# Kernel optimization log

Measured on AMD Instinct MI355X. Metric: run time of the kernel, lower is better.

The kernel has to match this reference:

```python
import jax, jax.numpy as jnp
import numpy as np

B = 4096          # number of instance groups (images)
C = 81            # num_classes + 1 (fixed by the 81x81 prior_rel buffer)
D_K = 64
MAX_N = 128       # max instances per group


def setup_inputs() -> dict:
    key = jax.random.key(0)
    rng = np.random.default_rng(0)
    ni = rng.integers(1, MAX_N + 1, size=B)
    ni[0] = MAX_N  # pin the max so padded length is deterministic
    num_instances = jnp.asarray(ni, dtype=jnp.int32)
    total = int(ni.sum())
    ks = jax.random.split(key, 10)
    s_in = 1.0 / np.sqrt(C)
    s_dk = 1.0 / np.sqrt(D_K)
    return {
        'x': jax.random.normal(ks[0], (total, C), jnp.float32),
        'num_instances': num_instances,
        'prior_rel': jax.random.normal(ks[1], (C, C), jnp.float32) * s_in,
        'wq': jax.random.normal(ks[2], (C, D_K), jnp.float32) * s_in,
        'bq': jnp.zeros((D_K,), jnp.float32),
        'wk': jax.random.normal(ks[3], (C, D_K), jnp.float32) * s_in,
        'bk': jnp.zeros((D_K,), jnp.float32),
        'wv': jax.random.normal(ks[4], (C, D_K), jnp.float32) * s_in,
        'bv': jnp.zeros((D_K,), jnp.float32),
        'wu': jax.random.normal(ks[5], (D_K, C), jnp.float32) * s_dk,
        'bu': jnp.zeros((C,), jnp.float32),
    }


def reference(x, num_instances, prior_rel, wq, bq, wk, bk, wv, bv, wu, bu):
    # num_instances is static ragged metadata (the torch code keeps it as a
    # Python list), so it is safe to pull concrete ints from it here.
    ni = np.asarray(num_instances)
    Bn = ni.shape[0]
    M = int(ni.max())
    total = x.shape[0]

    counts = jnp.asarray(ni, jnp.int32)                      # [B]
    offsets = jnp.concatenate([jnp.zeros((1,), jnp.int32),
                               jnp.cumsum(counts)[:-1]])      # [B]
    pos = jnp.arange(M, dtype=jnp.int32)                      # [M]
    mask = pos[None, :] < counts[:, None]                     # [B, M] valid slots
    idx = offsets[:, None] + pos[None, :]                     # [B, M] flat gather idx
    idx_safe = jnp.where(mask, idx, 0)

    # pad: split x into ragged groups, zero-pad each to length M
    padded = x[idx_safe] * mask[:, :, None].astype(x.dtype)   # [B, M, C]

    q = padded @ wq + bq                                      # [B, M, d_k]
    k = padded @ wk + bk                                      # [B, M, d_k]
    v = (padded @ prior_rel) @ wv + bv                        # [B, M, d_k]

    scores = jnp.einsum('bmd,bnd->bmn', q, k) / jnp.sqrt(
        jnp.asarray(D_K, x.dtype))                            # [B, M, M]
    # mask padded KEY columns (queries on padded rows are dropped at unpad)
    scores = jnp.where(mask[:, None, :], scores, -jnp.inf)
    probs = jax.nn.softmax(scores, axis=2)
    out = jnp.einsum('bmn,bnd->bmd', probs, v)                # [B, M, d_k]
    out = out @ wu + bu                                       # [B, M, C]

    # unpad: scatter valid rows back to their ragged flat positions
    tgt = jnp.where(mask, idx, total)                         # dump pad rows past end
    flat = jnp.zeros((total + 1, out.shape[-1]), out.dtype)
    flat = flat.at[tgt.reshape(-1)].set(out.reshape(-1, out.shape[-1]))
    return flat[:total]
```

## Files before the change

### kernel.cpp

```cpp
#include <hip/hip_runtime.h>


typedef __attribute__((ext_vector_type(8))) short short8;
typedef __attribute__((ext_vector_type(4))) float f32x4;
typedef __attribute__((ext_vector_type(4))) short short4v;

constexpr int C  = 81;
constexpr int DK = 64;
constexpr int CP = 96;

constexpr int QK_STRIDE = 72;
constexpr int VT_STRIDE = 136;
constexpr int OFF_K  = 0;
constexpr int OFF_VT = 128 * QK_STRIDE;
constexpr int SMEM_TOT = OFF_VT + 64 * VT_STRIDE;

__device__ inline ushort f2b(float f) {
    uint u = __float_as_uint(f);
    uint r = (u + 0x7fffu + ((u >> 16) & 1u)) >> 16;
    return (ushort)r;
}
__device__ inline uint pack2bf(float a, float b) {
    return (uint)f2b(a) | ((uint)f2b(b) << 16);
}
__device__ inline uint shflu(uint v, int srcLane) {
    return (uint)__shfl((int)v, srcLane, 64);
}
union U8 { short8 s; uint u[4]; };

#define MFMA16(a, b, c) __builtin_amdgcn_mfma_f32_16x16x32_bf16((a), (b), (c), 0, 0, 0)

__global__ void scan_counts(const int* __restrict__ counts,
                            int* __restrict__ offsets, int n) {
    __shared__ int part[256];
    int tid = threadIdx.x;
    int per = (n + 255) >> 8;
    int base = tid * per;
    int s = 0;
    for (int i = 0; i < per; i++) {
        int idx = base + i;
        if (idx < n) s += counts[idx];
    }
    part[tid] = s;
    __syncthreads();
    for (int off = 1; off < 256; off <<= 1) {
        int v = (tid >= off) ? part[tid - off] : 0;
        __syncthreads();
        part[tid] += v;
        __syncthreads();
    }
    int run = (tid == 0) ? 0 : part[tid - 1];
    for (int i = 0; i < per; i++) {
        int idx = base + i;
        if (idx < n) { offsets[idx] = run; run += counts[idx]; }
    }
}

__global__ void prep_weights(const float* __restrict__ prior,
                             const float* __restrict__ wq, const float* __restrict__ wk,
                             const float* __restrict__ wv, const float* __restrict__ wu,
                             ushort* __restrict__ wqT, ushort* __restrict__ wkT,
                             ushort* __restrict__ wvT, ushort* __restrict__ wuT) {
    int idx = blockIdx.x * 256 + threadIdx.x;
    int sec = idx / (DK * CP);
    int i   = idx - sec * (DK * CP);
    if (sec == 0 || sec == 1) {
        int n = i / CP, k = i - (i / CP) * CP;
        const float* w = (sec == 0) ? wq : wk;
        ushort* dst    = (sec == 0) ? wqT : wkT;
        dst[n * CP + k] = (k < C) ? f2b(w[k * DK + n]) : (ushort)0;
    } else if (sec == 2) {
        int n = i / CP, k = i - (i / CP) * CP;
        float s = 0.f;
        if (k < C)
            for (int e = 0; e < C; e++) s = fmaf(prior[k * C + e], wv[e * DK + n], s);
        wvT[n * CP + k] = (k < C) ? f2b(s) : (ushort)0;
    } else {
        int n = i / DK, k = i - (i / DK) * DK;
        wuT[n * DK + k] = (n < C) ? f2b(wu[k * C + n]) : (ushort)0;
    }
}

__launch_bounds__(256, 4)
__global__ void ravnet_mfma(const float* __restrict__ x,
                            const int* __restrict__ counts,
                            const int* __restrict__ offsets,
                            const ushort* __restrict__ wqT, const ushort* __restrict__ wkT,
                            const ushort* __restrict__ wvT, const ushort* __restrict__ wuT,
                            const float* __restrict__ bq, const float* __restrict__ bk,
                            const float* __restrict__ bv, const float* __restrict__ bu,
                            float* __restrict__ out) {
    __shared__ __align__(16) ushort sm[SMEM_TOT];

    const int b    = blockIdx.x;
    const int N    = counts[b];
    const long off = offsets[b];
    const int tid  = threadIdx.x;
    const int lane = tid & 63;
    const int wave = tid >> 6;
    const int quad = lane >> 4;
    const int m16  = lane & 15;
    const int NT8  = (N + 15) >> 4;
    const int NT4  = (N + 31) >> 5;
    const float* xsrc = x + off * C;

    const int srcE = ((quad & 1) << 5) + m16;
    const int srcO = srcE + 16;
    const bool hi  = (quad >> 1) != 0;

    short8 aq[2][2];

    #pragma unroll
    for (int t = 0; t < 2; t++) {
        const int rt = wave + 4 * t;
        if (rt < NT8) {
            const int row  = rt * 16 + m16;
            const bool vrow = row < N;
            const float* xr = xsrc + (long)(vrow ? row : (N - 1)) * C;
            short8 ax[3];
            #pragma unroll
            for (int ks = 0; ks < 2; ks++) {
                const int c0 = ks * 32 + quad * 8;
                short8 a;
                #pragma unroll
                for (int e = 0; e < 8; e++) a[e] = (short)f2b(vrow ? xr[c0 + e] : 0.f);
                ax[ks] = a;
            }
            {
                const int c0 = 64 + quad * 8;
                short8 a;
                #pragma unroll
                for (int e = 0; e < 8; e++) {
                    const int c = c0 + e;
                    a[e] = (short)((vrow && c < C) ? f2b(xr[c]) : (ushort)0);
                }
                ax[2] = a;
            }
            uint qpk[4][2];
            #pragma unroll
            for (int nt = 0; nt < 4; nt++) {
                f32x4 acc = {0.f, 0.f, 0.f, 0.f};
                #pragma unroll
                for (int ks = 0; ks < 3; ks++)
                    acc = MFMA16(*(const short8*)(wqT + (nt * 16 + m16) * CP + ks * 32 + quad * 8),
                                 ax[ks], acc);
                const f32x4 b4 = *(const f32x4*)(bq + nt * 16 + quad * 4);
                qpk[nt][0] = pack2bf(acc[0] + b4[0], acc[1] + b4[1]);
                qpk[nt][1] = pack2bf(acc[2] + b4[2], acc[3] + b4[3]);
            }
            #pragma unroll
            for (int ks = 0; ks < 2; ks++) {
                uint a0 = shflu(qpk[2 * ks][0], srcE), b0 = shflu(qpk[2 * ks + 1][0], srcE);
                uint a1 = shflu(qpk[2 * ks][1], srcE), b1 = shflu(qpk[2 * ks + 1][1], srcE);
                uint a2 = shflu(qpk[2 * ks][0], srcO), b2 = shflu(qpk[2 * ks + 1][0], srcO);
                uint a3 = shflu(qpk[2 * ks][1], srcO), b3 = shflu(qpk[2 * ks + 1][1], srcO);
                U8 u;
                u.u[0] = hi ? b0 : a0;  u.u[1] = hi ? b1 : a1;
                u.u[2] = hi ? b2 : a2;  u.u[3] = hi ? b3 : a3;
                aq[t][ks] = u.s;
            }
            #pragma unroll
            for (int nt = 0; nt < 4; nt++) {
                f32x4 acc = {0.f, 0.f, 0.f, 0.f};
                #pragma unroll
                for (int ks = 0; ks < 3; ks++)
                    acc = MFMA16(*(const short8*)(wkT + (nt * 16 + m16) * CP + ks * 32 + quad * 8),
                                 ax[ks], acc);
                const f32x4 b4 = *(const f32x4*)(bk + nt * 16 + quad * 4);
                short4v pk4;
                #pragma unroll
                for (int r = 0; r < 4; r++) pk4[r] = (short)f2b(acc[r] + b4[r]);
                *(short4v*)(sm + OFF_K + (rt * 16 + m16) * QK_STRIDE + nt * 16 + quad * 4) = pk4;
            }
            #pragma unroll
            for (int nt = 0; nt < 4; nt++) {
                f32x4 acc = {0.f, 0.f, 0.f, 0.f};
                #pragma unroll
                for (int ks = 0; ks < 3; ks++)
                    acc = MFMA16(ax[ks],
                                 *(const short8*)(wvT + (nt * 16 + m16) * CP + ks * 32 + quad * 8),
                                 acc);
                const float bb = bv[nt * 16 + m16];
                short4v pk4;
                #pragma unroll
                for (int r = 0; r < 4; r++) pk4[r] = (short)f2b(acc[r] + bb);
                *(short4v*)(sm + OFF_VT + (nt * 16 + m16) * VT_STRIDE + rt * 16 + quad * 4) = pk4;
            }
        }
    }
    if (NT8 & 1) {
        const int R = NT8 * 16;
        const int d = tid >> 2, c4 = (tid & 3) << 2;
        short4v z = {0, 0, 0, 0};
        *(short4v*)(sm + OFF_VT + d * VT_STRIDE + R + c4) = z;
    }
    __syncthreads();

    constexpr float SCALE = 0.18033688011112042f;
    #pragma unroll
    for (int t = 0; t < 2; t++) {
        const int qt = wave + 4 * t;
        if (qt < NT8) {
            f32x4 sacc[8];
            #pragma unroll
            for (int ct = 0; ct < 8; ct++) {
                if (ct < NT8) {
                    f32x4 a = {0.f, 0.f, 0.f, 0.f};
                    #pragma unroll
                    for (int ks = 0; ks < 2; ks++) {
                        short8 kb = *(const short8*)(sm + OFF_K + (ct * 16 + m16) * QK_STRIDE +
                                                     ks * 32 + quad * 8);
                        a = MFMA16(kb, aq[t][ks], a);
                    }
                    sacc[ct] = a;
                }
            }
            float mr = -3e38f;
            #pragma unroll
            for (int ct = 0; ct < 8; ct++) if (ct < NT8) {
                #pragma unroll
                for (int r = 0; r < 4; r++) {
                    const bool valid = (ct * 16 + quad * 4 + r) < N;
                    float s = valid ? sacc[ct][r] * SCALE : -3e38f;
                    sacc[ct][r] = s;
                    mr = fmaxf(mr, s);
                }
            }
            mr = fmaxf(mr, __shfl_xor(mr, 16, 64));
            mr = fmaxf(mr, __shfl_xor(mr, 32, 64));
            float lr = 0.f;
            #pragma unroll
            for (int ct = 0; ct < 8; ct++) if (ct < NT8) {
                #pragma unroll
                for (int r = 0; r < 4; r++) {
                    float p = __builtin_exp2f(sacc[ct][r] - mr);
                    sacc[ct][r] = p;
                    lr += p;
                }
            }
            lr += __shfl_xor(lr, 16, 64);
            lr += __shfl_xor(lr, 32, 64);
            const float linv = 1.f / lr;
            uint pk[8][2];
            #pragma unroll
            for (int ct = 0; ct < 8; ct++) {
                if (ct < NT8) {
                    pk[ct][0] = pack2bf(sacc[ct][0], sacc[ct][1]);
                    pk[ct][1] = pack2bf(sacc[ct][2], sacc[ct][3]);
                } else {
                    pk[ct][0] = 0u; pk[ct][1] = 0u;
                }
            }
            short8 ap[4];
            #pragma unroll
            for (int kt = 0; kt < 4; kt++) {
                if (kt < NT4) {
                    uint a0 = shflu(pk[2 * kt][0], srcE), b0 = shflu(pk[2 * kt + 1][0], srcE);
                    uint a1 = shflu(pk[2 * kt][1], srcE), b1 = shflu(pk[2 * kt + 1][1], srcE);
                    uint a2 = shflu(pk[2 * kt][0], srcO), b2 = shflu(pk[2 * kt + 1][0], srcO);
                    uint a3 = shflu(pk[2 * kt][1], srcO), b3 = shflu(pk[2 * kt + 1][1], srcO);
                    U8 u;
                    u.u[0] = hi ? b0 : a0;  u.u[1] = hi ? b1 : a1;
                    u.u[2] = hi ? b2 : a2;  u.u[3] = hi ? b3 : a3;
                    ap[kt] = u.s;
                }
            }
            uint opk[4][2];
            #pragma unroll
            for (int ot = 0; ot < 4; ot++) {
                f32x4 oa = {0.f, 0.f, 0.f, 0.f};
                #pragma unroll
                for (int kt = 0; kt < 4; kt++) if (kt < NT4) {
                    short8 vb = *(const short8*)(sm + OFF_VT + (ot * 16 + m16) * VT_STRIDE +
                                                 kt * 32 + quad * 8);
                    oa = MFMA16(vb, ap[kt], oa);
                }
                opk[ot][0] = pack2bf(oa[0] * linv, oa[1] * linv);
                opk[ot][1] = pack2bf(oa[2] * linv, oa[3] * linv);
            }
            short8 ao[2];
            #pragma unroll
            for (int ks = 0; ks < 2; ks++) {
                uint a0 = shflu(opk[2 * ks][0], srcE), b0 = shflu(opk[2 * ks + 1][0], srcE);
                uint a1 = shflu(opk[2 * ks][1], srcE), b1 = shflu(opk[2 * ks + 1][1], srcE);
                uint a2 = shflu(opk[2 * ks][0], srcO), b2 = shflu(opk[2 * ks + 1][0], srcO);
                uint a3 = shflu(opk[2 * ks][1], srcO), b3 = shflu(opk[2 * ks + 1][1], srcO);
                U8 u;
                u.u[0] = hi ? b0 : a0;  u.u[1] = hi ? b1 : a1;
                u.u[2] = hi ? b2 : a2;  u.u[3] = hi ? b3 : a3;
                ao[ks] = u.s;
            }
            const int row = qt * 16 + m16;
            #pragma unroll
            for (int ct = 0; ct < 6; ct++) {
                f32x4 acc = {0.f, 0.f, 0.f, 0.f};
                #pragma unroll
                for (int ks = 0; ks < 2; ks++) {
                    short8 wb = *(const short8*)(wuT + (ct * 16 + m16) * DK + ks * 32 + quad * 8);
                    acc = MFMA16(wb, ao[ks], acc);
                }
                if (row < N) {
                    #pragma unroll
                    for (int r = 0; r < 4; r++) {
                        const int e = ct * 16 + quad * 4 + r;
                        if (e < C) out[(off + row) * C + e] = acc[r] + bu[e];
                    }
                }
            }
        }
    }
}

extern "C" void kernel_launch(void* const* d_in, const int* in_sizes, int n_in,
                              void* d_out, int out_size, void* d_ws, size_t ws_size,
                              hipStream_t stream) {
    const float* x      = (const float*)d_in[0];
    const int*   counts = (const int*)  d_in[1];
    const float* prior  = (const float*)d_in[2];
    const float* wq     = (const float*)d_in[3];
    const float* bq     = (const float*)d_in[4];
    const float* wk     = (const float*)d_in[5];
    const float* bk     = (const float*)d_in[6];
    const float* wv     = (const float*)d_in[7];
    const float* bv     = (const float*)d_in[8];
    const float* wu     = (const float*)d_in[9];
    const float* bu     = (const float*)d_in[10];
    float* out = (float*)d_out;

    const int B = in_sizes[1];

    int*    offsets = (int*)d_ws;
    ushort* wqT = (ushort*)((char*)d_ws + (((size_t)B * sizeof(int) + 255) & ~(size_t)255));
    ushort* wkT = wqT + DK * CP;
    ushort* wvT = wkT + DK * CP;
    ushort* wuT = wvT + DK * CP;

    scan_counts<<<1, 256, 0, stream>>>(counts, offsets, B);
    prep_weights<<<(4 * DK * CP + 255) / 256, 256, 0, stream>>>(
        prior, wq, wk, wv, wu, wqT, wkT, wvT, wuT);
    ravnet_mfma<<<B, 256, 0, stream>>>(x, counts, offsets,
                                       wqT, wkT, wvT, wuT,
                                       bq, bk, bv, bu, out);
}
```

Measured before the change: 284.5 us.

## Swizzle LDS layout, hoist x loads, transpose output MFMA for coalesced stores

```diff
diff --git a/kernel.cpp b/kernel.cpp
--- a/kernel.cpp
+++ b/kernel.cpp
@@ -9,11 +9,16 @@
 constexpr int DK = 64;
 constexpr int CP = 96;
 
-constexpr int QK_STRIDE = 72;
-constexpr int VT_STRIDE = 136;
 constexpr int OFF_K  = 0;
-constexpr int OFF_VT = 128 * QK_STRIDE;
-constexpr int SMEM_TOT = OFF_VT + 64 * VT_STRIDE;
+constexpr int OFF_VT = 128 * 64;
+constexpr int SMEM_TOT = OFF_VT + 64 * 128;
+
+__device__ inline int kidx(int row, int colu) {
+    return OFF_K + row * 64 + (colu ^ ((row & 7) << 3));
+}
+__device__ inline int vidx(int dim, int colu) {
+    return OFF_VT + dim * 128 + (colu ^ ((dim & 15) << 3));
+}
 
 __device__ inline ushort f2b(float f) {
     uint u = __float_as_uint(f);
@@ -81,7 +86,7 @@
     }
 }
 
-__launch_bounds__(256, 4)
+__launch_bounds__(256, 5)
 __global__ void ravnet_mfma(const float* __restrict__ x,
                             const int* __restrict__ counts,
                             const int* __restrict__ offsets,
@@ -110,6 +115,7 @@
 
     short8 aq[2][2];
 
+    short8 ax2[2][3];
     #pragma unroll
     for (int t = 0; t < 2; t++) {
         const int rt = wave + 4 * t;
@@ -117,14 +123,13 @@
             const int row  = rt * 16 + m16;
             const bool vrow = row < N;
             const float* xr = xsrc + (long)(vrow ? row : (N - 1)) * C;
-            short8 ax[3];
             #pragma unroll
             for (int ks = 0; ks < 2; ks++) {
                 const int c0 = ks * 32 + quad * 8;
                 short8 a;
                 #pragma unroll
                 for (int e = 0; e < 8; e++) a[e] = (short)f2b(vrow ? xr[c0 + e] : 0.f);
-                ax[ks] = a;
+                ax2[t][ks] = a;
             }
             {
                 const int c0 = 64 + quad * 8;
@@ -134,8 +139,15 @@
                     const int c = c0 + e;
                     a[e] = (short)((vrow && c < C) ? f2b(xr[c]) : (ushort)0);
                 }
-                ax[2] = a;
-            }
+                ax2[t][2] = a;
+            }
+        }
+    }
+    #pragma unroll
+    for (int t = 0; t < 2; t++) {
+        const int rt = wave + 4 * t;
+        if (rt < NT8) {
+            const short8* ax = ax2[t];
             uint qpk[4][2];
             #pragma unroll
             for (int nt = 0; nt < 4; nt++) {
@@ -170,7 +182,7 @@
                 short4v pk4;
                 #pragma unroll
                 for (int r = 0; r < 4; r++) pk4[r] = (short)f2b(acc[r] + b4[r]);
-                *(short4v*)(sm + OFF_K + (rt * 16 + m16) * QK_STRIDE + nt * 16 + quad * 4) = pk4;
+                *(short4v*)(sm + kidx(rt * 16 + m16, nt * 16 + quad * 4)) = pk4;
             }
             #pragma unroll
             for (int nt = 0; nt < 4; nt++) {
@@ -184,7 +196,7 @@
                 short4v pk4;
                 #pragma unroll
                 for (int r = 0; r < 4; r++) pk4[r] = (short)f2b(acc[r] + bb);
-                *(short4v*)(sm + OFF_VT + (nt * 16 + m16) * VT_STRIDE + rt * 16 + quad * 4) = pk4;
+                *(short4v*)(sm + vidx(nt * 16 + m16, rt * 16 + quad * 4)) = pk4;
             }
         }
     }
@@ -192,11 +204,17 @@
         const int R = NT8 * 16;
         const int d = tid >> 2, c4 = (tid & 3) << 2;
         short4v z = {0, 0, 0, 0};
-        *(short4v*)(sm + OFF_VT + d * VT_STRIDE + R + c4) = z;
+        *(short4v*)(sm + vidx(d, R + c4)) = z;
     }
     __syncthreads();
 
     constexpr float SCALE = 0.18033688011112042f;
+    float bue[6];
+    #pragma unroll
+    for (int ct = 0; ct < 6; ct++) {
+        const int e = ct * 16 + m16;
+        bue[ct] = (e < C) ? bu[e] : 0.f;
+    }
     #pragma unroll
     for (int t = 0; t < 2; t++) {
         const int qt = wave + 4 * t;
@@ -208,8 +226,7 @@
                     f32x4 a = {0.f, 0.f, 0.f, 0.f};
                     #pragma unroll
                     for (int ks = 0; ks < 2; ks++) {
-                        short8 kb = *(const short8*)(sm + OFF_K + (ct * 16 + m16) * QK_STRIDE +
-                                                     ks * 32 + quad * 8);
+                        short8 kb = *(const short8*)(sm + kidx(ct * 16 + m16, ks * 32 + quad * 8));
                         a = MFMA16(kb, aq[t][ks], a);
                     }
                     sacc[ct] = a;
@@ -271,8 +288,7 @@
                 f32x4 oa = {0.f, 0.f, 0.f, 0.f};
                 #pragma unroll
                 for (int kt = 0; kt < 4; kt++) if (kt < NT4) {
-                    short8 vb = *(const short8*)(sm + OFF_VT + (ot * 16 + m16) * VT_STRIDE +
-                                                 kt * 32 + quad * 8);
+                    short8 vb = *(const short8*)(sm + vidx(ot * 16 + m16, kt * 32 + quad * 8));
                     oa = MFMA16(vb, ap[kt], oa);
                 }
                 opk[ot][0] = pack2bf(oa[0] * linv, oa[1] * linv);
@@ -290,20 +306,20 @@
                 u.u[2] = hi ? b2 : a2;  u.u[3] = hi ? b3 : a3;
                 ao[ks] = u.s;
             }
-            const int row = qt * 16 + m16;
             #pragma unroll
             for (int ct = 0; ct < 6; ct++) {
                 f32x4 acc = {0.f, 0.f, 0.f, 0.f};
                 #pragma unroll
                 for (int ks = 0; ks < 2; ks++) {
                     short8 wb = *(const short8*)(wuT + (ct * 16 + m16) * DK + ks * 32 + quad * 8);
-                    acc = MFMA16(wb, ao[ks], acc);
-                }
-                if (row < N) {
+                    acc = MFMA16(ao[ks], wb, acc);
+                }
+                const int e = ct * 16 + m16;
+                if (e < C) {
                     #pragma unroll
                     for (int r = 0; r < 4; r++) {
-                        const int e = ct * 16 + quad * 4 + r;
-                        if (e < C) out[(off + row) * C + e] = acc[r] + bu[e];
+                        const int row = qt * 16 + quad * 4 + r;
+                        if (row < N) out[(off + row) * C + e] = acc[r] + bue[ct];
                     }
                 }
             }
```

Measured after the change: 286.5 us. No clear change (+0.7%).
